# Kernel tuning notes

Hardware: AMD Instinct MI355X
Metric: run time of the kernel (lower is better)

## Reference

```python
import jax, jax.numpy as jnp
import numpy as np

N = 50000
E = 300000
D_IN = 256
D_OUT = 256


def setup_inputs() -> dict:
    key = jax.random.key(0)
    ks = jax.random.split(key, 9)
    obj_vecs = jax.random.normal(ks[0], (N, D_IN), dtype=jnp.float32)
    rel_vecs = jax.random.normal(ks[1], (N, D_IN), dtype=jnp.float32)
    edge_index = jax.random.randint(ks[2], (E, 2), 0, N, dtype=jnp.int64)
    s = 1.0 / np.sqrt(D_IN)
    # SAGEConv params: lin_l (applied to aggregated neighbors, with bias),
    # lin_r (applied to root/self features, no bias). One pair per conv.
    W_l_obj = jax.random.uniform(ks[3], (D_OUT, D_IN), minval=-s, maxval=s, dtype=jnp.float32)
    b_l_obj = jax.random.uniform(ks[4], (D_OUT,), minval=-s, maxval=s, dtype=jnp.float32)
    W_r_obj = jax.random.uniform(ks[5], (D_OUT, D_IN), minval=-s, maxval=s, dtype=jnp.float32)
    W_l_rel = jax.random.uniform(ks[6], (D_OUT, D_IN), minval=-s, maxval=s, dtype=jnp.float32)
    b_l_rel = jax.random.uniform(ks[7], (D_OUT,), minval=-s, maxval=s, dtype=jnp.float32)
    W_r_rel = jax.random.uniform(ks[8], (D_OUT, D_IN), minval=-s, maxval=s, dtype=jnp.float32)
    return {"obj_vecs": obj_vecs, "rel_vecs": rel_vecs, "edge_index": edge_index,
            "W_l_obj": W_l_obj, "b_l_obj": b_l_obj, "W_r_obj": W_r_obj,
            "W_l_rel": W_l_rel, "b_l_rel": b_l_rel, "W_r_rel": W_r_rel}


def _sage_conv(x, src, dst, W_l, b_l, W_r):
    # mean aggregation of source-node features at destination nodes
    msg = x[src]                                             # [E, D_IN] gather
    summed = jax.ops.segment_sum(msg, dst, num_segments=N)   # [N, D_IN]
    cnt = jax.ops.segment_sum(jnp.ones((src.shape[0],), x.dtype), dst, num_segments=N)
    agg = summed / jnp.maximum(cnt, 1.0)[:, None]
    # out = lin_l(agg) + lin_r(x)
    return agg @ W_l.T + b_l + x @ W_r.T


def reference(obj_vecs, rel_vecs, edge_index,
              W_l_obj, b_l_obj, W_r_obj, W_l_rel, b_l_rel, W_r_rel):
    # module transposes [E,2] -> [2,E]; PyG: messages flow src=row0 -> dst=row1
    src = edge_index[:, 0]
    dst = edge_index[:, 1]
    obj_out = _sage_conv(obj_vecs, src, dst, W_l_obj, b_l_obj, W_r_obj)
    rel_out = _sage_conv(rel_vecs, src, dst, W_l_rel, b_l_rel, W_r_rel)
    return (obj_out, rel_out)
```

## Files before the change

### kernel.cpp

```cpp
#include <hip/hip_runtime.h>

#define N_NODES 50000
#define N_EDGES 300000
#define DFEAT 256
#define KCAT 512
#define MT 16
#define APAD 8
#define AROW (KCAT + APAD)
#define NWELEM (KCAT * DFEAT)
#define CAP 32
#define XQ4 ((N_NODES * DFEAT) / 8)

typedef __attribute__((ext_vector_type(8))) short bf16x8;
typedef __attribute__((ext_vector_type(4))) float f32x4;

__device__ __forceinline__ unsigned short f2bf(float f) {
    union { float f; unsigned int u; } c; c.f = f;
    unsigned int r = c.u + 0x7FFF + ((c.u >> 16) & 1);
    return (unsigned short)(r >> 16);
}

__device__ __forceinline__ float bf2f(unsigned short u) {
    union { unsigned int i; float f; } c; c.i = (unsigned)u << 16; return c.f;
}

__global__ void k_xcast(const float* __restrict__ xo, const float* __restrict__ xr,
                        unsigned short* __restrict__ xbo, unsigned short* __restrict__ xbr,
                        int* __restrict__ cnt) {
    int id = blockIdx.x * blockDim.x + threadIdx.x;
    const float4* __restrict__ src;
    unsigned short* __restrict__ dst;
    int k;
    if (id < XQ4) { src = (const float4*)xo; dst = xbo; k = id; }
    else          { src = (const float4*)xr; dst = xbr; k = id - XQ4; }
    float4 a = src[2 * k], b = src[2 * k + 1];
    ushort4 u0 = make_ushort4(f2bf(a.x), f2bf(a.y), f2bf(a.z), f2bf(a.w));
    ushort4 u1 = make_ushort4(f2bf(b.x), f2bf(b.y), f2bf(b.z), f2bf(b.w));
    *(ushort4*)&dst[8 * k]     = u0;
    *(ushort4*)&dst[8 * k + 4] = u1;
    if (id < N_NODES) cnt[id] = 0;
}

__global__ void k_prep(const float* __restrict__ Wl_o, const float* __restrict__ Wr_o,
                       const float* __restrict__ Wl_r, const float* __restrict__ Wr_r,
                       unsigned short* __restrict__ Wb_o, unsigned short* __restrict__ Wb_r) {
    int id = blockIdx.x * blockDim.x + threadIdx.x;
    int wid  = id & (NWELEM - 1);
    int j    = wid & 7;
    int lane = (wid >> 3) & 63;
    int frag = wid >> 9;
    int nt   = frag & 15;
    int kb   = frag >> 4;
    int k = kb * 32 + (lane >> 4) * 8 + j;
    int n = nt * 16 + (lane & 15);
    if (id < NWELEM) {
        float v = (k < 256) ? Wl_o[n * 256 + k] : Wr_o[n * 256 + (k - 256)];
        Wb_o[wid] = f2bf(v);
    } else {
        float v = (k < 256) ? Wl_r[n * 256 + k] : Wr_r[n * 256 + (k - 256)];
        Wb_r[wid] = f2bf(v);
    }
}

__global__ void k_place(const long long* __restrict__ ei, int* __restrict__ cnt,
                        int* __restrict__ srcs2, int E) {
    int e = blockIdx.x * blockDim.x + threadIdx.x;
    if (e < E) {
        long long v = __builtin_nontemporal_load(&ei[e]);
        int s = (int)(v & 0xffffffffLL);
        int d = (int)(v >> 32);
        if ((unsigned)d < (unsigned)N_NODES) {
            int r = atomicAdd(&cnt[d], 1);
            if (r < CAP)
                srcs2[d * CAP + r] = ((unsigned)s < (unsigned)N_NODES) ? s : 0;
        }
    }
}

__global__ __launch_bounds__(256, 8)
void k_fused(const unsigned short* __restrict__ xb_obj, const unsigned short* __restrict__ xb_rel,
             const unsigned short* __restrict__ Wb_obj, const unsigned short* __restrict__ Wb_rel,
             const float* __restrict__ b_obj, const float* __restrict__ b_rel,
             const int* __restrict__ cnt, const int* __restrict__ srcs2,
             float* __restrict__ out, int n) {
    __shared__ unsigned short A[MT][AROW];

    const int tz = blockIdx.y;
    const unsigned short* __restrict__ xb = tz ? xb_rel : xb_obj;
    const unsigned short* __restrict__ Wb = tz ? Wb_rel : Wb_obj;
    const float* __restrict__ bia = tz ? b_rel : b_obj;
    float* __restrict__ outp = out + (size_t)tz * (size_t)N_NODES * DFEAT;

    const int t = threadIdx.x;
    const int wave = t >> 6, lane = t & 63;
    const int node0 = blockIdx.x * MT;

    const ushort4* __restrict__ xb4 = (const ushort4*)xb;
    for (int il = wave; il < MT; il += 4) {
        int node = node0 + il;
        float ax = 0.f, ay = 0.f, az = 0.f, aw = 0.f;
        ushort4 xv = make_ushort4(0, 0, 0, 0);
        float c = 0.f;
        if (node < n) {
            xv = xb4[(size_t)node * 64 + lane];
            int ecraw = cnt[node];
            if (ecraw < 0) ecraw = 0;
            int ec = (ecraw < CAP) ? ecraw : CAP;
            c = (float)ecraw;
            const int* __restrict__ sp = srcs2 + node * CAP;
            int e = 0;
            for (; e + 3 < ec; e += 4) {
                int s0 = sp[e], s1 = sp[e + 1], s2 = sp[e + 2], s3 = sp[e + 3];
                ushort4 v0 = xb4[(size_t)s0 * 64 + lane];
                ushort4 v1 = xb4[(size_t)s1 * 64 + lane];
                ushort4 v2 = xb4[(size_t)s2 * 64 + lane];
                ushort4 v3 = xb4[(size_t)s3 * 64 + lane];
                ax += (bf2f(v0.x) + bf2f(v1.x)) + (bf2f(v2.x) + bf2f(v3.x));
                ay += (bf2f(v0.y) + bf2f(v1.y)) + (bf2f(v2.y) + bf2f(v3.y));
                az += (bf2f(v0.z) + bf2f(v1.z)) + (bf2f(v2.z) + bf2f(v3.z));
                aw += (bf2f(v0.w) + bf2f(v1.w)) + (bf2f(v2.w) + bf2f(v3.w));
            }
            if (e + 1 < ec) {
                int s0 = sp[e], s1 = sp[e + 1];
                ushort4 v0 = xb4[(size_t)s0 * 64 + lane];
                ushort4 v1 = xb4[(size_t)s1 * 64 + lane];
                ax += bf2f(v0.x) + bf2f(v1.x); ay += bf2f(v0.y) + bf2f(v1.y);
                az += bf2f(v0.z) + bf2f(v1.z); aw += bf2f(v0.w) + bf2f(v1.w);
                e += 2;
            }
            if (e < ec) {
                int s0 = sp[e];
                ushort4 v = xb4[(size_t)s0 * 64 + lane];
                ax += bf2f(v.x); ay += bf2f(v.y); az += bf2f(v.z); aw += bf2f(v.w);
            }
            float inv = 1.0f / fmaxf(c, 1.0f);
            ax *= inv; ay *= inv; az *= inv; aw *= inv;
        }
        ushort4 a16 = make_ushort4(f2bf(ax), f2bf(ay), f2bf(az), f2bf(aw));
        *(ushort4*)&A[il][4 * lane]       = a16;
        *(ushort4*)&A[il][256 + 4 * lane] = xv;
    }
    __syncthreads();

    const int nt0 = wave * 4;
    const int lq  = lane >> 4;
    const int lm  = lane & 15;

    f32x4 acc[4];
    #pragma unroll
    for (int ct = 0; ct < 4; ct++) {
        float b = bia[(nt0 + ct) * 16 + lm];
        acc[ct] = (f32x4){b, b, b, b};
    }

    const bf16x8* __restrict__ Wb8 = (const bf16x8*)Wb;
    #pragma unroll
    for (int kb = 0; kb < 16; kb++) {
        bf16x8 af = *(const bf16x8*)&A[lm][kb * 32 + lq * 8];
        #pragma unroll
        for (int ct = 0; ct < 4; ct++) {
            bf16x8 bf = Wb8[(size_t)(kb * 16 + nt0 + ct) * 64 + lane];
            acc[ct] = __builtin_amdgcn_mfma_f32_16x16x32_bf16(af, bf, acc[ct], 0, 0, 0);
        }
    }

    #pragma unroll
    for (int ct = 0; ct < 4; ct++) {
        int col = (nt0 + ct) * 16 + lm;
        #pragma unroll
        for (int r = 0; r < 4; r++) {
            int node = node0 + lq * 4 + r;
            if (node < n) outp[((size_t)node << 8) + col] = acc[ct][r];
        }
    }
}

extern "C" void kernel_launch(void* const* d_in, const int* in_sizes, int n_in,
                              void* d_out, int out_size, void* d_ws, size_t ws_size,
                              hipStream_t stream) {
    const float*     obj  = (const float*)d_in[0];
    const float*     rel  = (const float*)d_in[1];
    const long long* ei   = (const long long*)d_in[2];
    const float*     Wl_o = (const float*)d_in[3];
    const float*     bl_o = (const float*)d_in[4];
    const float*     Wr_o = (const float*)d_in[5];
    const float*     Wl_r = (const float*)d_in[6];
    const float*     bl_r = (const float*)d_in[7];
    const float*     Wr_r = (const float*)d_in[8];
    float* out = (float*)d_out;

    char* w = (char*)d_ws;
    size_t o = 0;
    auto alloc = [&](size_t b) { size_t r = o; o += (b + 255) & ~(size_t)255; return r; };
    int*            cnt    = (int*)(w + alloc((size_t)N_NODES * 4));
    int*            srcs2  = (int*)(w + alloc((size_t)N_NODES * CAP * 4));
    unsigned short* Wb_o   = (unsigned short*)(w + alloc((size_t)NWELEM * 2));
    unsigned short* Wb_r   = (unsigned short*)(w + alloc((size_t)NWELEM * 2));
    unsigned short* xb_o   = (unsigned short*)(w + alloc((size_t)N_NODES * DFEAT * 2));
    unsigned short* xb_r   = (unsigned short*)(w + alloc((size_t)N_NODES * DFEAT * 2));

    k_xcast<<<(2 * XQ4 + 255) / 256, 256, 0, stream>>>(obj, rel, xb_o, xb_r, cnt);
    k_prep<<<(2 * NWELEM) / 256, 256, 0, stream>>>(Wl_o, Wr_o, Wl_r, Wr_r, Wb_o, Wb_r);
    k_place<<<(N_EDGES + 255) / 256, 256, 0, stream>>>(ei, cnt, srcs2, N_EDGES);

    dim3 g((N_NODES + MT - 1) / MT, 2);
    k_fused<<<g, 256, 0, stream>>>(xb_o, xb_r, Wb_o, Wb_r, bl_o, bl_r, cnt, srcs2, out, N_NODES);
}
```

Before: 309.6 us.

## Interleave obj/rel bf16 features per node and fuse both convs per block

```diff
diff --git a/kernel.cpp b/kernel.cpp
--- a/kernel.cpp
+++ b/kernel.cpp
@@ -4,7 +4,7 @@
 #define N_EDGES 300000
 #define DFEAT 256
 #define KCAT 512
-#define MT 16
+#define MT 8
 #define APAD 8
 #define AROW (KCAT + APAD)
 #define NWELEM (KCAT * DFEAT)
@@ -13,6 +13,7 @@
 
 typedef __attribute__((ext_vector_type(8))) short bf16x8;
 typedef __attribute__((ext_vector_type(4))) float f32x4;
+typedef __attribute__((ext_vector_type(8))) unsigned short ushort8;
 
 __device__ __forceinline__ unsigned short f2bf(float f) {
     union { float f; unsigned int u; } c; c.f = f;
@@ -25,19 +26,20 @@
 }
 
 __global__ void k_xcast(const float* __restrict__ xo, const float* __restrict__ xr,
-                        unsigned short* __restrict__ xbo, unsigned short* __restrict__ xbr,
-                        int* __restrict__ cnt) {
+                        unsigned short* __restrict__ xbb, int* __restrict__ cnt) {
     int id = blockIdx.x * blockDim.x + threadIdx.x;
-    const float4* __restrict__ src;
-    unsigned short* __restrict__ dst;
-    int k;
-    if (id < XQ4) { src = (const float4*)xo; dst = xbo; k = id; }
-    else          { src = (const float4*)xr; dst = xbr; k = id - XQ4; }
-    float4 a = src[2 * k], b = src[2 * k + 1];
+    int isrel = (id >= XQ4);
+    int k = isrel ? (id - XQ4) : id;
+    const f32x4* __restrict__ src = (const f32x4*)(isrel ? xr : xo);
+    f32x4 a = __builtin_nontemporal_load(&src[2 * k]);
+    f32x4 b = __builtin_nontemporal_load(&src[2 * k + 1]);
+    int node = k >> 5;
+    int ch   = k & 31;
+    unsigned short* dst = xbb + (size_t)node * 512 + (isrel ? 256 : 0) + ch * 8;
     ushort4 u0 = make_ushort4(f2bf(a.x), f2bf(a.y), f2bf(a.z), f2bf(a.w));
     ushort4 u1 = make_ushort4(f2bf(b.x), f2bf(b.y), f2bf(b.z), f2bf(b.w));
-    *(ushort4*)&dst[8 * k]     = u0;
-    *(ushort4*)&dst[8 * k + 4] = u1;
+    *(ushort4*)dst       = u0;
+    *(ushort4*)(dst + 4) = u1;
     if (id < N_NODES) cnt[id] = 0;
 }
 
@@ -78,31 +80,28 @@
 }
 
 __global__ __launch_bounds__(256, 8)
-void k_fused(const unsigned short* __restrict__ xb_obj, const unsigned short* __restrict__ xb_rel,
+void k_fused(const unsigned short* __restrict__ xbb,
              const unsigned short* __restrict__ Wb_obj, const unsigned short* __restrict__ Wb_rel,
              const float* __restrict__ b_obj, const float* __restrict__ b_rel,
              const int* __restrict__ cnt, const int* __restrict__ srcs2,
              float* __restrict__ out, int n) {
-    __shared__ unsigned short A[MT][AROW];
-
-    const int tz = blockIdx.y;
-    const unsigned short* __restrict__ xb = tz ? xb_rel : xb_obj;
-    const unsigned short* __restrict__ Wb = tz ? Wb_rel : Wb_obj;
-    const float* __restrict__ bia = tz ? b_rel : b_obj;
-    float* __restrict__ outp = out + (size_t)tz * (size_t)N_NODES * DFEAT;
+    __shared__ unsigned short A_o[MT][AROW];
+    __shared__ unsigned short A_r[MT][AROW];
 
     const int t = threadIdx.x;
     const int wave = t >> 6, lane = t & 63;
     const int node0 = blockIdx.x * MT;
 
-    const ushort4* __restrict__ xb4 = (const ushort4*)xb;
+    const ushort8* __restrict__ xb8 = (const ushort8*)xbb;
     for (int il = wave; il < MT; il += 4) {
         int node = node0 + il;
-        float ax = 0.f, ay = 0.f, az = 0.f, aw = 0.f;
-        ushort4 xv = make_ushort4(0, 0, 0, 0);
+        float a8[8];
+        #pragma unroll
+        for (int j = 0; j < 8; j++) a8[j] = 0.f;
+        ushort8 xv = (ushort8)0;
         float c = 0.f;
         if (node < n) {
-            xv = xb4[(size_t)node * 64 + lane];
+            xv = xb8[(size_t)node * 64 + lane];
             int ecraw = cnt[node];
             if (ecraw < 0) ecraw = 0;
             int ec = (ecraw < CAP) ? ecraw : CAP;
@@ -111,66 +110,79 @@
             int e = 0;
             for (; e + 3 < ec; e += 4) {
                 int s0 = sp[e], s1 = sp[e + 1], s2 = sp[e + 2], s3 = sp[e + 3];
-                ushort4 v0 = xb4[(size_t)s0 * 64 + lane];
-                ushort4 v1 = xb4[(size_t)s1 * 64 + lane];
-                ushort4 v2 = xb4[(size_t)s2 * 64 + lane];
-                ushort4 v3 = xb4[(size_t)s3 * 64 + lane];
-                ax += (bf2f(v0.x) + bf2f(v1.x)) + (bf2f(v2.x) + bf2f(v3.x));
-                ay += (bf2f(v0.y) + bf2f(v1.y)) + (bf2f(v2.y) + bf2f(v3.y));
-                az += (bf2f(v0.z) + bf2f(v1.z)) + (bf2f(v2.z) + bf2f(v3.z));
-                aw += (bf2f(v0.w) + bf2f(v1.w)) + (bf2f(v2.w) + bf2f(v3.w));
+                ushort8 v0 = xb8[(size_t)s0 * 64 + lane];
+                ushort8 v1 = xb8[(size_t)s1 * 64 + lane];
+                ushort8 v2 = xb8[(size_t)s2 * 64 + lane];
+                ushort8 v3 = xb8[(size_t)s3 * 64 + lane];
+                #pragma unroll
+                for (int j = 0; j < 8; j++)
+                    a8[j] += (bf2f(v0[j]) + bf2f(v1[j])) + (bf2f(v2[j]) + bf2f(v3[j]));
             }
             if (e + 1 < ec) {
                 int s0 = sp[e], s1 = sp[e + 1];
-                ushort4 v0 = xb4[(size_t)s0 * 64 + lane];
-                ushort4 v1 = xb4[(size_t)s1 * 64 + lane];
-                ax += bf2f(v0.x) + bf2f(v1.x); ay += bf2f(v0.y) + bf2f(v1.y);
-                az += bf2f(v0.z) + bf2f(v1.z); aw += bf2f(v0.w) + bf2f(v1.w);
+                ushort8 v0 = xb8[(size_t)s0 * 64 + lane];
+                ushort8 v1 = xb8[(size_t)s1 * 64 + lane];
+                #pragma unroll
+                for (int j = 0; j < 8; j++) a8[j] += bf2f(v0[j]) + bf2f(v1[j]);
                 e += 2;
             }
             if (e < ec) {
                 int s0 = sp[e];
-                ushort4 v = xb4[(size_t)s0 * 64 + lane];
-                ax += bf2f(v.x); ay += bf2f(v.y); az += bf2f(v.z); aw += bf2f(v.w);
+                ushort8 v = xb8[(size_t)s0 * 64 + lane];
+                #pragma unroll
+                for (int j = 0; j < 8; j++) a8[j] += bf2f(v[j]);
             }
             float inv = 1.0f / fmaxf(c, 1.0f);
-            ax *= inv; ay *= inv; az *= inv; aw *= inv;
-        }
-        ushort4 a16 = make_ushort4(f2bf(ax), f2bf(ay), f2bf(az), f2bf(aw));
-        *(ushort4*)&A[il][4 * lane]       = a16;
-        *(ushort4*)&A[il][256 + 4 * lane] = xv;
+            #pragma unroll
+            for (int j = 0; j < 8; j++) a8[j] *= inv;
+        }
+        ushort8 agg;
+        #pragma unroll
+        for (int j = 0; j < 8; j++) agg[j] = f2bf(a8[j]);
+        int half = lane & 31;
+        unsigned short* base = (lane < 32) ? &A_o[il][0] : &A_r[il][0];
+        *(ushort8*)&base[8 * half]       = agg;
+        *(ushort8*)&base[256 + 8 * half] = xv;
     }
     __syncthreads();
 
-    const int nt0 = wave * 4;
-    const int lq  = lane >> 4;
-    const int lm  = lane & 15;
-
-    f32x4 acc[4];
+    const int conv = wave >> 1;
+    const int nth  = (wave & 1) * 8;
+    const unsigned short (*At)[AROW] = conv ? A_r : A_o;
+    const unsigned short* __restrict__ Wb = conv ? Wb_rel : Wb_obj;
+    const float* __restrict__ bia = conv ? b_rel : b_obj;
+    float* __restrict__ outp = out + (size_t)conv * (size_t)N_NODES * DFEAT;
+
+    const int lq = lane >> 4;
+    const int lm = lane & 15;
+
+    f32x4 acc[8];
     #pragma unroll
-    for (int ct = 0; ct < 4; ct++) {
-        float b = bia[(nt0 + ct) * 16 + lm];
+    for (int ct = 0; ct < 8; ct++) {
+        float b = bia[(nth + ct) * 16 + lm];
         acc[ct] = (f32x4){b, b, b, b};
     }
 
     const bf16x8* __restrict__ Wb8 = (const bf16x8*)Wb;
     #pragma unroll
     for (int kb = 0; kb < 16; kb++) {
-        bf16x8 af = *(const bf16x8*)&A[lm][kb * 32 + lq * 8];
-        #pragma unroll
-        for (int ct = 0; ct < 4; ct++) {
-            bf16x8 bf = Wb8[(size_t)(kb * 16 + nt0 + ct) * 64 + lane];
+        bf16x8 af = *(const bf16x8*)&At[lm & 7][kb * 32 + lq * 8];
+        #pragma unroll
+        for (int ct = 0; ct < 8; ct++) {
+            bf16x8 bf = Wb8[(size_t)(kb * 16 + nth + ct) * 64 + lane];
             acc[ct] = __builtin_amdgcn_mfma_f32_16x16x32_bf16(af, bf, acc[ct], 0, 0, 0);
         }
     }
 
-    #pragma unroll
-    for (int ct = 0; ct < 4; ct++) {
-        int col = (nt0 + ct) * 16 + lm;
-        #pragma unroll
-        for (int r = 0; r < 4; r++) {
-            int node = node0 + lq * 4 + r;
-            if (node < n) outp[((size_t)node << 8) + col] = acc[ct][r];
+    if (lq < 2) {
+        #pragma unroll
+        for (int ct = 0; ct < 8; ct++) {
+            int col = (nth + ct) * 16 + lm;
+            #pragma unroll
+            for (int r = 0; r < 4; r++) {
+                int node = node0 + lq * 4 + r;
+                if (node < n) outp[((size_t)node << 8) + col] = acc[ct][r];
+            }
         }
     }
 }
@@ -196,13 +208,12 @@
     int*            srcs2  = (int*)(w + alloc((size_t)N_NODES * CAP * 4));
     unsigned short* Wb_o   = (unsigned short*)(w + alloc((size_t)NWELEM * 2));
     unsigned short* Wb_r   = (unsigned short*)(w + alloc((size_t)NWELEM * 2));
-    unsigned short* xb_o   = (unsigned short*)(w + alloc((size_t)N_NODES * DFEAT * 2));
-    unsigned short* xb_r   = (unsigned short*)(w + alloc((size_t)N_NODES * DFEAT * 2));
-
-    k_xcast<<<(2 * XQ4 + 255) / 256, 256, 0, stream>>>(obj, rel, xb_o, xb_r, cnt);
+    unsigned short* xbb    = (unsigned short*)(w + alloc((size_t)N_NODES * KCAT * 2));
+
+    k_xcast<<<(2 * XQ4 + 255) / 256, 256, 0, stream>>>(obj, rel, xbb, cnt);
     k_prep<<<(2 * NWELEM) / 256, 256, 0, stream>>>(Wl_o, Wr_o, Wl_r, Wr_r, Wb_o, Wb_r);
     k_place<<<(N_EDGES + 255) / 256, 256, 0, stream>>>(ei, cnt, srcs2, N_EDGES);
 
-    dim3 g((N_NODES + MT - 1) / MT, 2);
-    k_fused<<<g, 256, 0, stream>>>(xb_o, xb_r, Wb_o, Wb_r, bl_o, bl_r, cnt, srcs2, out, N_NODES);
-}
+    k_fused<<<(N_NODES + MT - 1) / MT, 256, 0, stream>>>(xbb, Wb_o, Wb_r, bl_o, bl_r,
+                                                         cnt, srcs2, out, N_NODES);
+}
```

Result: slower. 400.3 us (+29.3%).

## Merge preprocessing kernels into one launch and interleave two-node gathers

Applied to the files above, without the earlier changes.

```diff
diff --git a/kernel.cpp b/kernel.cpp
--- a/kernel.cpp
+++ b/kernel.cpp
@@ -10,6 +10,9 @@
 #define NWELEM (KCAT * DFEAT)
 #define CAP 32
 #define XQ4 ((N_NODES * DFEAT) / 8)
+#define XCAST_BLKS ((2 * XQ4) / 256)
+#define PLACE_BLKS ((N_EDGES + 255) / 256)
+#define PREP_BLKS  ((2 * NWELEM) / 256)
 
 typedef __attribute__((ext_vector_type(8))) short bf16x8;
 typedef __attribute__((ext_vector_type(4))) float f32x4;
@@ -24,55 +27,55 @@
     union { unsigned int i; float f; } c; c.i = (unsigned)u << 16; return c.f;
 }
 
-__global__ void k_xcast(const float* __restrict__ xo, const float* __restrict__ xr,
-                        unsigned short* __restrict__ xbo, unsigned short* __restrict__ xbr,
-                        int* __restrict__ cnt) {
-    int id = blockIdx.x * blockDim.x + threadIdx.x;
-    const float4* __restrict__ src;
-    unsigned short* __restrict__ dst;
-    int k;
-    if (id < XQ4) { src = (const float4*)xo; dst = xbo; k = id; }
-    else          { src = (const float4*)xr; dst = xbr; k = id - XQ4; }
-    float4 a = src[2 * k], b = src[2 * k + 1];
-    ushort4 u0 = make_ushort4(f2bf(a.x), f2bf(a.y), f2bf(a.z), f2bf(a.w));
-    ushort4 u1 = make_ushort4(f2bf(b.x), f2bf(b.y), f2bf(b.z), f2bf(b.w));
-    *(ushort4*)&dst[8 * k]     = u0;
-    *(ushort4*)&dst[8 * k + 4] = u1;
-    if (id < N_NODES) cnt[id] = 0;
-}
-
-__global__ void k_prep(const float* __restrict__ Wl_o, const float* __restrict__ Wr_o,
-                       const float* __restrict__ Wl_r, const float* __restrict__ Wr_r,
-                       unsigned short* __restrict__ Wb_o, unsigned short* __restrict__ Wb_r) {
-    int id = blockIdx.x * blockDim.x + threadIdx.x;
-    int wid  = id & (NWELEM - 1);
-    int j    = wid & 7;
-    int lane = (wid >> 3) & 63;
-    int frag = wid >> 9;
-    int nt   = frag & 15;
-    int kb   = frag >> 4;
-    int k = kb * 32 + (lane >> 4) * 8 + j;
-    int n = nt * 16 + (lane & 15);
-    if (id < NWELEM) {
-        float v = (k < 256) ? Wl_o[n * 256 + k] : Wr_o[n * 256 + (k - 256)];
-        Wb_o[wid] = f2bf(v);
+__global__ void k_pre(const float* __restrict__ xo, const float* __restrict__ xr,
+                      unsigned short* __restrict__ xbo, unsigned short* __restrict__ xbr,
+                      const long long* __restrict__ ei, int* __restrict__ cnt,
+                      int* __restrict__ srcs2,
+                      const float* __restrict__ Wl_o, const float* __restrict__ Wr_o,
+                      const float* __restrict__ Wl_r, const float* __restrict__ Wr_r,
+                      unsigned short* __restrict__ Wb_o, unsigned short* __restrict__ Wb_r) {
+    int b = blockIdx.x, t = threadIdx.x;
+    if (b < XCAST_BLKS) {
+        int id = b * 256 + t;
+        const f32x4* __restrict__ src;
+        unsigned short* __restrict__ dst;
+        int k;
+        if (id < XQ4) { src = (const f32x4*)xo; dst = xbo; k = id; }
+        else          { src = (const f32x4*)xr; dst = xbr; k = id - XQ4; }
+        f32x4 a = __builtin_nontemporal_load(&src[2 * k]);
+        f32x4 bb = __builtin_nontemporal_load(&src[2 * k + 1]);
+        ushort4 u0 = make_ushort4(f2bf(a.x), f2bf(a.y), f2bf(a.z), f2bf(a.w));
+        ushort4 u1 = make_ushort4(f2bf(bb.x), f2bf(bb.y), f2bf(bb.z), f2bf(bb.w));
+        *(ushort4*)&dst[8 * k]     = u0;
+        *(ushort4*)&dst[8 * k + 4] = u1;
+    } else if (b < XCAST_BLKS + PLACE_BLKS) {
+        int e = (b - XCAST_BLKS) * 256 + t;
+        if (e < N_EDGES) {
+            long long v = __builtin_nontemporal_load(&ei[e]);
+            int s = (int)(v & 0xffffffffLL);
+            int d = (int)(v >> 32);
+            if ((unsigned)d < (unsigned)N_NODES) {
+                int r = atomicAdd(&cnt[d], 1);
+                if (r < CAP)
+                    srcs2[d * CAP + r] = ((unsigned)s < (unsigned)N_NODES) ? s : 0;
+            }
+        }
     } else {
-        float v = (k < 256) ? Wl_r[n * 256 + k] : Wr_r[n * 256 + (k - 256)];
-        Wb_r[wid] = f2bf(v);
-    }
-}
-
-__global__ void k_place(const long long* __restrict__ ei, int* __restrict__ cnt,
-                        int* __restrict__ srcs2, int E) {
-    int e = blockIdx.x * blockDim.x + threadIdx.x;
-    if (e < E) {
-        long long v = __builtin_nontemporal_load(&ei[e]);
-        int s = (int)(v & 0xffffffffLL);
-        int d = (int)(v >> 32);
-        if ((unsigned)d < (unsigned)N_NODES) {
-            int r = atomicAdd(&cnt[d], 1);
-            if (r < CAP)
-                srcs2[d * CAP + r] = ((unsigned)s < (unsigned)N_NODES) ? s : 0;
+        int id = (b - XCAST_BLKS - PLACE_BLKS) * 256 + t;
+        int wid  = id & (NWELEM - 1);
+        int j    = wid & 7;
+        int lane = (wid >> 3) & 63;
+        int frag = wid >> 9;
+        int nt   = frag & 15;
+        int kb   = frag >> 4;
+        int k = kb * 32 + (lane >> 4) * 8 + j;
+        int n = nt * 16 + (lane & 15);
+        if (id < NWELEM) {
+            float v = (k < 256) ? Wl_o[n * 256 + k] : Wr_o[n * 256 + (k - 256)];
+            Wb_o[wid] = f2bf(v);
+        } else {
+            float v = (k < 256) ? Wl_r[n * 256 + k] : Wr_r[n * 256 + (k - 256)];
+            Wb_r[wid] = f2bf(v);
         }
     }
 }
@@ -82,7 +85,7 @@
              const unsigned short* __restrict__ Wb_obj, const unsigned short* __restrict__ Wb_rel,
              const float* __restrict__ b_obj, const float* __restrict__ b_rel,
              const int* __restrict__ cnt, const int* __restrict__ srcs2,
-             float* __restrict__ out, int n) {
+             float* __restrict__ out) {
     __shared__ unsigned short A[MT][AROW];
 
     const int tz = blockIdx.y;
@@ -96,49 +99,82 @@
     const int node0 = blockIdx.x * MT;
 
     const ushort4* __restrict__ xb4 = (const ushort4*)xb;
-    for (int il = wave; il < MT; il += 4) {
-        int node = node0 + il;
-        float ax = 0.f, ay = 0.f, az = 0.f, aw = 0.f;
-        ushort4 xv = make_ushort4(0, 0, 0, 0);
-        float c = 0.f;
-        if (node < n) {
-            xv = xb4[(size_t)node * 64 + lane];
-            int ecraw = cnt[node];
-            if (ecraw < 0) ecraw = 0;
-            int ec = (ecraw < CAP) ? ecraw : CAP;
-            c = (float)ecraw;
-            const int* __restrict__ sp = srcs2 + node * CAP;
-            int e = 0;
-            for (; e + 3 < ec; e += 4) {
-                int s0 = sp[e], s1 = sp[e + 1], s2 = sp[e + 2], s3 = sp[e + 3];
-                ushort4 v0 = xb4[(size_t)s0 * 64 + lane];
-                ushort4 v1 = xb4[(size_t)s1 * 64 + lane];
-                ushort4 v2 = xb4[(size_t)s2 * 64 + lane];
-                ushort4 v3 = xb4[(size_t)s3 * 64 + lane];
-                ax += (bf2f(v0.x) + bf2f(v1.x)) + (bf2f(v2.x) + bf2f(v3.x));
-                ay += (bf2f(v0.y) + bf2f(v1.y)) + (bf2f(v2.y) + bf2f(v3.y));
-                az += (bf2f(v0.z) + bf2f(v1.z)) + (bf2f(v2.z) + bf2f(v3.z));
-                aw += (bf2f(v0.w) + bf2f(v1.w)) + (bf2f(v2.w) + bf2f(v3.w));
-            }
-            if (e + 1 < ec) {
-                int s0 = sp[e], s1 = sp[e + 1];
-                ushort4 v0 = xb4[(size_t)s0 * 64 + lane];
-                ushort4 v1 = xb4[(size_t)s1 * 64 + lane];
-                ax += bf2f(v0.x) + bf2f(v1.x); ay += bf2f(v0.y) + bf2f(v1.y);
-                az += bf2f(v0.z) + bf2f(v1.z); aw += bf2f(v0.w) + bf2f(v1.w);
-                e += 2;
-            }
-            if (e < ec) {
-                int s0 = sp[e];
-                ushort4 v = xb4[(size_t)s0 * 64 + lane];
-                ax += bf2f(v.x); ay += bf2f(v.y); az += bf2f(v.z); aw += bf2f(v.w);
-            }
-            float inv = 1.0f / fmaxf(c, 1.0f);
-            ax *= inv; ay *= inv; az *= inv; aw *= inv;
-        }
-        ushort4 a16 = make_ushort4(f2bf(ax), f2bf(ay), f2bf(az), f2bf(aw));
-        *(ushort4*)&A[il][4 * lane]       = a16;
-        *(ushort4*)&A[il][256 + 4 * lane] = xv;
+
+    auto tail = [&](float* a, const int* __restrict__ sp, int e, int ec) {
+        while (e + 3 < ec) {
+            int4 i4 = *(const int4*)&sp[e];
+            ushort4 v0 = xb4[(size_t)i4.x * 64 + lane];
+            ushort4 v1 = xb4[(size_t)i4.y * 64 + lane];
+            ushort4 v2 = xb4[(size_t)i4.z * 64 + lane];
+            ushort4 v3 = xb4[(size_t)i4.w * 64 + lane];
+            a[0] += (bf2f(v0.x) + bf2f(v1.x)) + (bf2f(v2.x) + bf2f(v3.x));
+            a[1] += (bf2f(v0.y) + bf2f(v1.y)) + (bf2f(v2.y) + bf2f(v3.y));
+            a[2] += (bf2f(v0.z) + bf2f(v1.z)) + (bf2f(v2.z) + bf2f(v3.z));
+            a[3] += (bf2f(v0.w) + bf2f(v1.w)) + (bf2f(v2.w) + bf2f(v3.w));
+            e += 4;
+        }
+        if (e + 1 < ec) {
+            int s0 = sp[e], s1 = sp[e + 1];
+            ushort4 v0 = xb4[(size_t)s0 * 64 + lane];
+            ushort4 v1 = xb4[(size_t)s1 * 64 + lane];
+            a[0] += bf2f(v0.x) + bf2f(v1.x); a[1] += bf2f(v0.y) + bf2f(v1.y);
+            a[2] += bf2f(v0.z) + bf2f(v1.z); a[3] += bf2f(v0.w) + bf2f(v1.w);
+            e += 2;
+        }
+        if (e < ec) {
+            int s0 = sp[e];
+            ushort4 v = xb4[(size_t)s0 * 64 + lane];
+            a[0] += bf2f(v.x); a[1] += bf2f(v.y); a[2] += bf2f(v.z); a[3] += bf2f(v.w);
+        }
+    };
+
+    #pragma unroll
+    for (int half = 0; half < 2; ++half) {
+        const int ilA = wave + 8 * half, ilB = ilA + 4;
+        const int nodeA = node0 + ilA,  nodeB = node0 + ilB;
+        ushort4 xvA = xb4[(size_t)nodeA * 64 + lane];
+        ushort4 xvB = xb4[(size_t)nodeB * 64 + lane];
+        int cA = cnt[nodeA]; if (cA < 0) cA = 0;
+        int cB = cnt[nodeB]; if (cB < 0) cB = 0;
+        int ecA = (cA < CAP) ? cA : CAP;
+        int ecB = (cB < CAP) ? cB : CAP;
+        const int* __restrict__ spA = srcs2 + nodeA * CAP;
+        const int* __restrict__ spB = srcs2 + nodeB * CAP;
+        float aA[4] = {0.f, 0.f, 0.f, 0.f}, aB[4] = {0.f, 0.f, 0.f, 0.f};
+        int eA = 0, eB = 0;
+        while (eA + 3 < ecA && eB + 3 < ecB) {
+            int4 iA = *(const int4*)&spA[eA];
+            int4 iB = *(const int4*)&spB[eB];
+            ushort4 vA0 = xb4[(size_t)iA.x * 64 + lane];
+            ushort4 vA1 = xb4[(size_t)iA.y * 64 + lane];
+            ushort4 vA2 = xb4[(size_t)iA.z * 64 + lane];
+            ushort4 vA3 = xb4[(size_t)iA.w * 64 + lane];
+            ushort4 vB0 = xb4[(size_t)iB.x * 64 + lane];
+            ushort4 vB1 = xb4[(size_t)iB.y * 64 + lane];
+            ushort4 vB2 = xb4[(size_t)iB.z * 64 + lane];
+            ushort4 vB3 = xb4[(size_t)iB.w * 64 + lane];
+            aA[0] += (bf2f(vA0.x) + bf2f(vA1.x)) + (bf2f(vA2.x) + bf2f(vA3.x));
+            aA[1] += (bf2f(vA0.y) + bf2f(vA1.y)) + (bf2f(vA2.y) + bf2f(vA3.y));
+            aA[2] += (bf2f(vA0.z) + bf2f(vA1.z)) + (bf2f(vA2.z) + bf2f(vA3.z));
+            aA[3] += (bf2f(vA0.w) + bf2f(vA1.w)) + (bf2f(vA2.w) + bf2f(vA3.w));
+            aB[0] += (bf2f(vB0.x) + bf2f(vB1.x)) + (bf2f(vB2.x) + bf2f(vB3.x));
+            aB[1] += (bf2f(vB0.y) + bf2f(vB1.y)) + (bf2f(vB2.y) + bf2f(vB3.y));
+            aB[2] += (bf2f(vB0.z) + bf2f(vB1.z)) + (bf2f(vB2.z) + bf2f(vB3.z));
+            aB[3] += (bf2f(vB0.w) + bf2f(vB1.w)) + (bf2f(vB2.w) + bf2f(vB3.w));
+            eA += 4; eB += 4;
+        }
+        tail(aA, spA, eA, ecA);
+        tail(aB, spB, eB, ecB);
+        float invA = 1.0f / fmaxf((float)cA, 1.0f);
+        float invB = 1.0f / fmaxf((float)cB, 1.0f);
+        ushort4 gA = make_ushort4(f2bf(aA[0] * invA), f2bf(aA[1] * invA),
+                                  f2bf(aA[2] * invA), f2bf(aA[3] * invA));
+        ushort4 gB = make_ushort4(f2bf(aB[0] * invB), f2bf(aB[1] * invB),
+                                  f2bf(aB[2] * invB), f2bf(aB[3] * invB));
+        *(ushort4*)&A[ilA][4 * lane]       = gA;
+        *(ushort4*)&A[ilA][256 + 4 * lane] = xvA;
+        *(ushort4*)&A[ilB][4 * lane]       = gB;
+        *(ushort4*)&A[ilB][256 + 4 * lane] = xvB;
     }
     __syncthreads();
 
@@ -170,7 +206,7 @@
         #pragma unroll
         for (int r = 0; r < 4; r++) {
             int node = node0 + lq * 4 + r;
-            if (node < n) outp[((size_t)node << 8) + col] = acc[ct][r];
+            outp[((size_t)node << 8) + col] = acc[ct][r];
         }
     }
 }
@@ -199,10 +235,10 @@
     unsigned short* xb_o   = (unsigned short*)(w + alloc((size_t)N_NODES * DFEAT * 2));
     unsigned short* xb_r   = (unsigned short*)(w + alloc((size_t)N_NODES * DFEAT * 2));
 
-    k_xcast<<<(2 * XQ4 + 255) / 256, 256, 0, stream>>>(obj, rel, xb_o, xb_r, cnt);
-    k_prep<<<(2 * NWELEM) / 256, 256, 0, stream>>>(Wl_o, Wr_o, Wl_r, Wr_r, Wb_o, Wb_r);
-    k_place<<<(N_EDGES + 255) / 256, 256, 0, stream>>>(ei, cnt, srcs2, N_EDGES);
-
-    dim3 g((N_NODES + MT - 1) / MT, 2);
-    k_fused<<<g, 256, 0, stream>>>(xb_o, xb_r, Wb_o, Wb_r, bl_o, bl_r, cnt, srcs2, out, N_NODES);
-}
+    hipMemsetAsync(cnt, 0, (size_t)N_NODES * 4, stream);
+    k_pre<<<XCAST_BLKS + PLACE_BLKS + PREP_BLKS, 256, 0, stream>>>(
+        obj, rel, xb_o, xb_r, ei, cnt, srcs2, Wl_o, Wr_o, Wl_r, Wr_r, Wb_o, Wb_r);
+
+    dim3 g(N_NODES / MT, 2);
+    k_fused<<<g, 256, 0, stream>>>(xb_o, xb_r, Wb_o, Wb_r, bl_o, bl_r, cnt, srcs2, out);
+}
```

Result: no change. 305.4 us (-1.3%).
